# Kernel tuning notes

Hardware: AMD Instinct MI355X
Metric: run time of the kernel (lower is better)

The kernel has to match this reference:

```python
import jax, jax.numpy as jnp
import numpy as np

B, NUM_CLASSES, G = 8, 80, 100
IMG = 1280
STRIDES = (8, 16, 32)
EPS = 1e-7            # mmyolo EPS in -log(iou + EPS)
IOU_EPS = 1e-6        # BboxOverlaps2D union eps
INF = 1e8
SOFT_CENTER_RADIUS = 3.0
TOPK = 13
IOU_WEIGHT = 3.0


def _make_priors():
    ps = []
    for s in STRIDES:
        n = IMG // s
        c = (jnp.arange(n, dtype=jnp.float32) + 0.5) * s
        yy, xx = jnp.meshgrid(c, c, indexing='ij')
        st = jnp.full((n * n,), float(s), jnp.float32)
        ps.append(jnp.stack([xx.ravel(), yy.ravel(), st, st], axis=-1))
    return jnp.concatenate(ps, axis=0)  # [N, 4] = (cx, cy, stride_x, stride_y)


def setup_inputs() -> dict:
    key = jax.random.key(0)
    k = jax.random.split(key, 8)
    priors = _make_priors()
    N = priors.shape[0]  # 33600
    # predicted boxes jittered around anchor points, xyxy
    cxcy = priors[None, :, :2] + jax.random.normal(k[0], (B, N, 2)) * priors[None, :, 2:3] * 2.0
    wh = priors[None, :, 2:3] * (1.0 + 4.0 * jax.random.uniform(k[1], (B, N, 2)))
    pred_bboxes = jnp.concatenate([cxcy - wh / 2, cxcy + wh / 2], axis=-1)
    pred_scores = jax.random.normal(k[2], (B, N, NUM_CLASSES)) * 2.0 - 2.0  # logits
    # gt boxes inside the image, xyxy
    x1y1 = jax.random.uniform(k[3], (B, G, 2)) * (IMG - 200)
    gwh = 20.0 + jax.random.uniform(k[4], (B, G, 2)) * 180.0
    gt_bboxes = jnp.concatenate([x1y1, x1y1 + gwh], axis=-1)
    gt_labels = jax.random.randint(k[5], (B, G, 1), 0, NUM_CLASSES)
    counts = jax.random.randint(k[6], (B,), 10, G + 1)
    pad_bbox_flag = (jnp.arange(G)[None, :] < counts[:, None]).astype(jnp.float32)[..., None]
    return {"pred_bboxes": pred_bboxes, "pred_scores": pred_scores, "priors": priors,
            "gt_labels": gt_labels, "gt_bboxes": gt_bboxes, "pad_bbox_flag": pad_bbox_flag}


def _pairwise_iou(b1, b2):
    # b1 [B,N,4], b2 [B,G,4] in xyxy -> [B,N,G]
    a1 = (b1[..., 2] - b1[..., 0]) * (b1[..., 3] - b1[..., 1])
    a2 = (b2[..., 2] - b2[..., 0]) * (b2[..., 3] - b2[..., 1])
    lt = jnp.maximum(b1[:, :, None, :2], b2[:, None, :, :2])
    rb = jnp.minimum(b1[:, :, None, 2:], b2[:, None, :, 2:])
    wh = jnp.clip(rb - lt, 0.0)
    overlap = wh[..., 0] * wh[..., 1]
    union = a1[:, :, None] + a2[:, None, :] - overlap
    return overlap / jnp.maximum(union, IOU_EPS)


def reference(pred_bboxes, pred_scores, priors, gt_labels, gt_bboxes, pad_bbox_flag):
    Bb, N, _ = pred_bboxes.shape
    Gg = gt_bboxes.shape[1]
    centers = priors[:, :2]
    valid_gt = pad_bbox_flag[..., 0] > 0  # [B,G]

    # point-in-box test (strict >0, as in find_inside_points)
    lt = centers[None, :, None, :] - gt_bboxes[:, None, :, :2]   # [B,N,G,2]
    rb = gt_bboxes[:, None, :, 2:] - centers[None, :, None, :]
    is_in = (jnp.minimum(jnp.min(lt, -1), jnp.min(rb, -1)) > 0) & valid_gt[:, None, :]
    valid_mask = jnp.any(is_in, -1)  # [B,N]

    # soft center prior
    gt_center = (gt_bboxes[..., :2] + gt_bboxes[..., 2:]) / 2.0
    strides = priors[:, 2]
    dist = jnp.sqrt(jnp.sum((centers[None, :, None, :] - gt_center[:, None, :, :]) ** 2, -1))
    dist = dist / strides[None, :, None] * valid_mask[..., None].astype(dist.dtype)
    soft_center_prior = jnp.power(10.0, dist - SOFT_CENTER_RADIUS)

    # IoU cost
    ious = _pairwise_iou(pred_bboxes, gt_bboxes)  # [B,N,G]
    iou_cost = -jnp.log(ious + EPS) * IOU_WEIGHT

    # classification cost: gather pred score of each gt's class
    lbl = jnp.broadcast_to(gt_labels[:, None, :, 0], (Bb, N, Gg))
    x = jnp.take_along_axis(pred_scores, lbl, axis=2)  # logits [B,N,G]
    scale = ious - jax.nn.sigmoid(x)
    bce = jax.nn.softplus(x) - x * ious  # BCE-with-logits, target=ious
    cls_cost = bce * (scale * scale)

    cost = cls_cost + iou_cost + soft_center_prior
    cost = jnp.where(valid_mask[..., None], cost, INF)

    # dynamic k per gt = clamp(int(sum of top-13 ious), min 1)
    k = min(TOPK, N)
    topk_ious = jax.lax.top_k(jnp.swapaxes(ious, 1, 2), k)[0]  # [B,G,k]
    dyn_k = jnp.maximum(jnp.sum(topk_ious, -1).astype(jnp.int32), 1)  # [B,G]

    # rank of each prior's cost within its gt column (ascending)
    ranks = jnp.argsort(jnp.argsort(cost, axis=1), axis=1)
    matching = (ranks < dyn_k[:, None, :]) & valid_gt[:, None, :]  # [B,N,G]

    # resolve priors matched to multiple gts: keep min-cost gt
    multi = jnp.sum(matching, -1) > 1  # [B,N]
    argmin_g = jnp.argmin(cost, axis=-1)
    onehot = argmin_g[..., None] == jnp.arange(Gg)[None, None, :]
    matching = jnp.where(multi[..., None], onehot, matching)

    fg = jnp.any(matching, -1)                       # [B,N]
    matched_gt = jnp.argmax(matching, -1)            # [B,N]
    matched_ious = jnp.sum(jnp.where(matching, ious, 0.0), -1)

    lbls = jnp.take_along_axis(gt_labels[..., 0], matched_gt, axis=1)
    assigned_labels = jnp.where(fg, lbls, NUM_CLASSES)
    assigned_labels_weights = jnp.ones((Bb, N), pred_scores.dtype)
    boxes = jnp.take_along_axis(gt_bboxes, matched_gt[..., None], axis=1)
    assigned_bboxes = jnp.where(fg[..., None], boxes, 0.0)
    assign_metrics = jnp.where(fg, matched_ious, 0.0)
    return assigned_labels, assigned_labels_weights, assigned_bboxes, assign_metrics
```

## Files before the change

kernel.cpp:

```cpp
#include <hip/hip_runtime.h>
#include <stdint.h>

#define BDIM 256
#define TDIM 512
#define B_   8
#define NCLS 80
#define G_   100
#define N_   33600
#define TOPK_ 13
#define TILES 525
#define NW   8
#define CAPC 160
#define CAPI 160
#define INFC 1e8f


__device__ __forceinline__ unsigned int fkey(float f){
  unsigned int u = __float_as_uint(f);
  return (u & 0x80000000u) ? ~u : (u | 0x80000000u);
}
__device__ __forceinline__ float unfkey(unsigned int k){
  unsigned int u = (k & 0x80000000u) ? (k & 0x7fffffffu) : ~k;
  return __uint_as_float(u);
}

__device__ __forceinline__ float cost_eval(float iou, float x, float dist, bool valid){
  #pragma clang fp contract(off)
  float prior = exp2f((dist - 3.0f) * 3.321928094887362f);
  float iouc  = -logf(iou + 1e-7f) * 3.0f;
  float sig   = 1.0f / (1.0f + expf(-x));
  float sc    = iou - sig;
  float bce   = fmaxf(x, 0.0f) + log1pf(expf(-fabsf(x))) - x * iou;
  float c     = bce * (sc * sc) + iouc + prior;
  return valid ? c : INFC;
}

__device__ __forceinline__ unsigned long long wave_min_u64(unsigned long long v){
  #pragma unroll
  for (int m = 1; m < 64; m <<= 1){
    unsigned int lo = (unsigned int)__shfl_xor((int)(unsigned int)v, m, 64);
    unsigned int hi = (unsigned int)__shfl_xor((int)(unsigned int)(v >> 32), m, 64);
    unsigned long long o = ((unsigned long long)hi << 32) | lo;
    v = o < v ? o : v;
  }
  return v;
}

__device__ __forceinline__ void tile_params(int t, int& W, int& base, int& trow, int& tcol,
                                            float& s, float& invs){
  if (t < 400){            W = 160; base = 0;     s = 8.0f;  invs = 0.125f;
    trow = (t/20)*8;  tcol = (t - (t/20)*20)*8; }
  else if (t < 500){ int u = t - 400; W = 80; base = 25600; s = 16.0f; invs = 0.0625f;
    trow = (u/10)*8; tcol = (u - (u/10)*10)*8; }
  else {             int u = t - 500; W = 40; base = 32000; s = 32.0f; invs = 0.03125f;
    trow = (u/5)*8;  tcol = (u - (u/5)*5)*8; }
}

__device__ unsigned long long compact_cost(unsigned long long* buf, int cnt){
  const int lane = threadIdx.x & 63;
  unsigned long long a0 = (lane       < cnt) ? buf[lane]       : ~0ull;
  unsigned long long a1 = (lane + 64  < cnt) ? buf[lane + 64]  : ~0ull;
  unsigned long long a2 = (lane + 128 < cnt) ? buf[lane + 128] : ~0ull;
  unsigned long long mykeep = ~0ull, t13 = ~0ull;
  #pragma unroll
  for (int r = 0; r < TOPK_; ++r){
    unsigned long long v = a0 < a1 ? a0 : a1; v = v < a2 ? v : a2;
    unsigned long long mn = wave_min_u64(v);
    if      (a0 == mn) a0 = ~0ull;
    else if (a1 == mn) a1 = ~0ull;
    else if (a2 == mn) a2 = ~0ull;
    if (lane == r) mykeep = mn;
    t13 = mn;
  }
  if (lane < TOPK_) buf[lane] = mykeep;
  return t13;
}

__device__ float compact_iou(float* buf, int cnt){
  const int lane = threadIdx.x & 63;
  float a0 = (lane       < cnt) ? buf[lane]       : -1.0f;
  float a1 = (lane + 64  < cnt) ? buf[lane + 64]  : -1.0f;
  float a2 = (lane + 128 < cnt) ? buf[lane + 128] : -1.0f;
  float mykeep = -1.0f, t13 = -1.0f;
  #pragma unroll
  for (int r = 0; r < TOPK_; ++r){
    float mx = fmaxf(fmaxf(a0, a1), a2);
    #pragma unroll
    for (int m = 1; m < 64; m <<= 1) mx = fmaxf(mx, __shfl_xor(mx, m, 64));
    bool h0 = (a0 == mx), h1 = (a1 == mx), h2 = (a2 == mx);
    unsigned long long ball = __ballot(h0 | h1 | h2);
    int src = (int)(__ffsll(ball) - 1);
    if (lane == src){
      if (h0) a0 = -1.0f; else if (h1) a1 = -1.0f; else a2 = -1.0f;
    }
    if (lane == r) mykeep = mx;
    t13 = mx;
  }
  if (lane < TOPK_) buf[lane] = mykeep;
  return t13;
}


__global__ void __launch_bounds__(64) k_prep(
    const float* __restrict__ pred_bboxes,
    const float* __restrict__ gt_bboxes,
    const float* __restrict__ pad_flag,
    unsigned char* __restrict__ valid_mask,
    uint32_t* __restrict__ match_mask,
    float4* __restrict__ tile_agg,
    uint32_t* __restrict__ tile_flag)
{
  const int t = blockIdx.x, b = blockIdx.y, l = threadIdx.x;
  __shared__ float4 sbox[G_];
  __shared__ float  sflag[G_];
  for (int g = l; g < G_; g += 64){
    sbox[g]  = ((const float4*)gt_bboxes)[b*G_ + g];
    sflag[g] = pad_flag[b*G_ + g];
  }
  __syncthreads();

  int W, base, trow, tcol; float s, invs;
  tile_params(t, W, base, trow, tcol, s, invs);
  int row = trow + (l >> 3), col = tcol + (l & 7);
  int n = base + row*W + col;
  float cx = ((float)col + 0.5f)*s, cy = ((float)row + 0.5f)*s;

  bool v = false;
  for (int g = 0; g < G_; ++g){
    float4 gb = sbox[g];
    bool in = (cx - gb.x > 0.0f) & (cy - gb.y > 0.0f) &
              (gb.z - cx > 0.0f) & (gb.w - cy > 0.0f) & (sflag[g] > 0.0f);
    v |= in;
  }
  size_t idx = (size_t)b*N_ + n;
  valid_mask[idx] = v ? 1 : 0;
  ((uint4*)match_mask)[idx] = make_uint4(0u,0u,0u,0u);

  float4 pb = ((const float4*)pred_bboxes)[idx];
  float x1 = pb.x, y1 = pb.y, x2 = pb.z, y2 = pb.w;
  #pragma unroll
  for (int m = 1; m < 64; m <<= 1){
    x1 = fminf(x1, __shfl_xor(x1, m, 64));
    y1 = fminf(y1, __shfl_xor(y1, m, 64));
    x2 = fmaxf(x2, __shfl_xor(x2, m, 64));
    y2 = fmaxf(y2, __shfl_xor(y2, m, 64));
  }
  unsigned long long anyb = __ballot(v);
  if (l == 0){
    tile_agg [(size_t)b*TILES + t] = make_float4(x1, y1, x2, y2);
    tile_flag[(size_t)b*TILES + t] = (anyb != 0ull) ? 1u : 0u;
  }
}


__global__ void __launch_bounds__(TDIM) k_topk(
    const float* __restrict__ pred_bboxes,
    const float* __restrict__ pred_scores,
    const int*   __restrict__ gt_labels,
    const float* __restrict__ gt_bboxes,
    const float* __restrict__ pad_flag,
    const unsigned char* __restrict__ valid_mask,
    const float4* __restrict__ tile_agg,
    const uint32_t* __restrict__ tile_flag,
    uint32_t* __restrict__ match_mask)
{
  #pragma clang fp contract(off)
  const int g = blockIdx.x, b = blockIdx.y;
  if (pad_flag[b*G_ + g] <= 0.0f) return;

  __shared__ unsigned long long s_cbuf[NW][CAPC];
  __shared__ float s_ibuf[NW][CAPI];
  __shared__ unsigned long long s_fk[NW*TOPK_];
  __shared__ float s_fi[NW*TOPK_];
  __shared__ float s_thr[2];

  const int tid = threadIdx.x, lane = tid & 63, wid = tid >> 6;
  unsigned long long* cbuf = s_cbuf[wid];
  float* ibuf = s_ibuf[wid];

  const float4 gb = ((const float4*)gt_bboxes)[b*G_ + g];
  const float ga  = (gb.z - gb.x) * (gb.w - gb.y);
  const float gcx = (gb.x + gb.z) * 0.5f, gcy = (gb.y + gb.w) * 0.5f;
  const int lbl = gt_labels[b*G_ + g];
  const unsigned int KEYINF = fkey(INFC);

  const float4* pb4 = (const float4*)pred_bboxes + (size_t)b*N_;
  const unsigned char* vm = valid_mask + (size_t)b*N_;
  const float* sc_b = pred_scores + (size_t)b*N_*NCLS;
  const float4* tag = tile_agg + (size_t)b*TILES;
  const uint32_t* tfl = tile_flag + (size_t)b*TILES;

  if (wid == 0){
    auto seed_eval = [&](int t, float& cst, float& iouv){
      #pragma clang fp contract(off)
      int nk, bs; float s, invs;
      if      (t < 25){ nk = 160; bs = 0;     s = 8.0f;  invs = 0.125f;   }
      else if (t < 50){ nk = 80;  bs = 25600; s = 16.0f; invs = 0.0625f;  }
      else            { nk = 40;  bs = 32000; s = 32.0f; invs = 0.03125f; }
      int rem = (t < 25) ? t : ((t < 50) ? t - 25 : t - 50);
      int r = rem / 5, c = rem - 5*r;
      int ix = (int)(gcx / s) - 2, iy = (int)(gcy / s) - 2;
      ix = ix < 0 ? 0 : (ix > nk-5 ? nk-5 : ix);
      iy = iy < 0 ? 0 : (iy > nk-5 ? nk-5 : iy);
      int col = ix + c, row = iy + r;
      int n = bs + row*nk + col;
      float4 pb = pb4[n];
      float pa = (pb.z - pb.x) * (pb.w - pb.y);
      float lx = fmaxf(pb.x, gb.x), ly = fmaxf(pb.y, gb.y);
      float rx = fminf(pb.z, gb.z), ry = fminf(pb.w, gb.w);
      float ov = fmaxf(rx - lx, 0.0f) * fmaxf(ry - ly, 0.0f);
      float un = pa + ga - ov;
      float iou = ov / fmaxf(un, 1e-6f);
      iouv = iou;
      bool valid = vm[n] != 0;
      float px = ((float)col + 0.5f)*s, py = ((float)row + 0.5f)*s;
      float dx = px - gcx, dy = py - gcy;
      float dist = sqrtf(dx*dx + dy*dy) * invs;
      float x = valid ? sc_b[(size_t)n*NCLS + lbl] : 0.0f;
      cst = cost_eval(iou, x, dist, valid);
    };
    float c0 = 3e38f, c1 = 3e38f, i0 = -1.0f, i1 = -1.0f;
    seed_eval(lane, c0, i0);
    if (lane < 11) seed_eval(lane + 64, c1, i1);
    float T = INFC;
    {
      const float lvs[7] = {47.0f, 24.0f, 12.0f, 6.0f, 3.0f, 1.5f, 0.75f};
      #pragma unroll
      for (int i = 0; i < 7; ++i){
        int cnt = __popcll(__ballot(c0 <= lvs[i])) + __popcll(__ballot(c1 <= lvs[i]));
        if (cnt >= TOPK_) T = lvs[i];
      }
    }
    float Ti = 0.0f;
    {
      const float ivs[8] = {0.02f, 0.05f, 0.1f, 0.15f, 0.22f, 0.3f, 0.4f, 0.5f};
      #pragma unroll
      for (int i = 0; i < 8; ++i){
        int cnt = __popcll(__ballot(i0 >= ivs[i])) + __popcll(__ballot(i1 >= ivs[i]));
        if (cnt >= TOPK_) Ti = ivs[i] * 0.999f;
      }
    }
    if (lane == 0){ s_thr[0] = T; s_thr[1] = Ti; }
  }
  __syncthreads();

  const float T0 = s_thr[0];
  float Tiou_m = s_thr[1];
  unsigned long long Tkey = ((unsigned long long)fkey(T0) << 32) | 0xFFFFFFFFull;
  bool  tc48  = T0 < 48.0f;
  float gt_   = 3.02f + log10f(T0);
  float gthr2 = gt_ * gt_;

  int ccnt = 0, icnt = 0;

  int sweep_nend = 0;
  if (T0 == INFC){
    int found = 0, base = 0;
    while (found < TOPK_ && base < N_){
      int n = base + lane;
      bool inv = (vm[n] == 0);
      unsigned long long m = __ballot(inv);
      int pc = __popcll(m);
      if (wid == 0){
        int pos = ccnt + (int)__popcll(m & ((1ull << lane) - 1ull));
        if (inv) cbuf[pos] = ((unsigned long long)KEYINF << 32) | (unsigned)n;
        ccnt += pc;
      }
      found += pc;
      base += 64;
    }
    sweep_nend = base;
  }

  const int per  = (TILES + NW - 1) / NW;
  const int lo_w = wid*per;
  const int hi_w = min(TILES, lo_w + per);

  for (int tb = lo_w; tb < hi_w; tb += 64){
    int tt2 = tb + lane;
    bool pass = false;
    if (tt2 < hi_w){
      float4 ag = tag[tt2];
      uint32_t fl2 = tfl[tt2];
      int W, bse, trow, tcol; float s, invs;
      tile_params(tt2, W, bse, trow, tcol, s, invs);
      bool inter = (fminf(ag.z, gb.z) > fmaxf(ag.x, gb.x)) &&
                   (fminf(ag.w, gb.w) > fmaxf(ag.y, gb.y));
      float rx0 = ((float)tcol + 0.5f)*s, rx1 = ((float)tcol + 7.5f)*s;
      float ry0 = ((float)trow + 0.5f)*s, ry1 = ((float)trow + 7.5f)*s;
      float ddx = fmaxf(0.0f, fmaxf(rx0 - gcx, gcx - rx1));
      float ddy = fmaxf(0.0f, fmaxf(ry0 - gcy, gcy - ry1));
      float md2s = (ddx*ddx + ddy*ddy) * (invs*invs);
      bool costok = (fl2 != 0) && (md2s <= gthr2) && (inter || !tc48);
      pass = inter || costok;
    }
    unsigned long long pm = __ballot(pass);
    while (pm){
      int bit = (int)(__ffsll(pm) - 1);
      pm &= pm - 1ull;
      const int tt = tb + bit;

      int W, bse, trow, tcol; float s, invs;
      tile_params(tt, W, bse, trow, tcol, s, invs);
      int row = trow + (lane >> 3), col = tcol + (lane & 7);
      int n = bse + row*W + col;
      float px = ((float)col + 0.5f)*s, py = ((float)row + 0.5f)*s;
      float4 pb = pb4[n];
      float pa = (pb.z - pb.x) * (pb.w - pb.y);
      float lx = fmaxf(pb.x, gb.x), ly = fmaxf(pb.y, gb.y);
      float rx = fminf(pb.z, gb.z), ry = fminf(pb.w, gb.w);
      float ov = fmaxf(rx - lx, 0.0f) * fmaxf(ry - ly, 0.0f);
      float un = pa + ga - ov;
      bool ipass = ov > Tiou_m * un;

      float dx = px - gcx, dy = py - gcy;
      float dist2 = dx*dx + dy*dy;
      float d2s = dist2 * (invs * invs);
      bool valid = vm[n] != 0;
      bool needcost = valid && (d2s <= gthr2) && !((ov <= 0.0f) && tc48);

      float iou = 0.0f;
      if (__any(ipass || needcost)){
        if (ipass || needcost) iou = ov / fmaxf(un, 1e-6f);
      }

      {
        unsigned long long m = __ballot(ipass);
        if (m){
          int pc = __popcll(m);
          if (icnt + pc > CAPI){
            float t = compact_iou(ibuf, icnt); icnt = TOPK_;
            Tiou_m = t * 0.999f;
          }
          int pos = icnt + (int)__popcll(m & ((1ull << lane) - 1ull));
          if (ipass) ibuf[pos] = iou;
          icnt += pc;
        }
      }

      unsigned long long key = ((unsigned long long)KEYINF << 32) | (unsigned)n;
      bool cpass = (!valid) && (key < Tkey) && (n >= sweep_nend);
      if (__any(needcost)){
        if (needcost){
          float x = sc_b[(size_t)n*NCLS + lbl];
          float dist = sqrtf(dist2) * invs;
          float c = cost_eval(iou, x, dist, true);
          key = ((unsigned long long)fkey(c) << 32) | (unsigned)n;
          cpass = key < Tkey;
        }
      }
      {
        unsigned long long m = __ballot(cpass);
        if (m){
          int pc = __popcll(m);
          if (ccnt + pc > CAPC){
            Tkey = compact_cost(cbuf, ccnt); ccnt = TOPK_;
            float Tc = unfkey((unsigned int)(Tkey >> 32));
            tc48 = Tc < 48.0f;
            float gq = 3.02f + log10f(Tc);
            gthr2 = (gq > 0.0f) ? gq*gq : 1e30f;
          }
          int pos = ccnt + (int)__popcll(m & ((1ull << lane) - 1ull));
          if (cpass) cbuf[pos] = key;
          ccnt += pc;
        }
      }
    }
  }

  compact_cost(cbuf, ccnt);
  compact_iou(ibuf, icnt);
  if (lane < TOPK_){ s_fk[wid*TOPK_ + lane] = cbuf[lane]; s_fi[wid*TOPK_ + lane] = ibuf[lane]; }
  __syncthreads();

  if (wid == 0){
    compact_cost(s_fk, NW*TOPK_);
    compact_iou(s_fi, NW*TOPK_);
  }
  __syncthreads();

  if (tid == 0){
    float ssum = 0.0f;
    for (int r = 0; r < TOPK_; ++r) ssum += fmaxf(s_fi[r], 0.0f);
    int dynk = (int)ssum;
    if (dynk < 1) dynk = 1;
    if (dynk > TOPK_) dynk = TOPK_;
    for (int r = 0; r < dynk; ++r){
      int n = (int)(s_fk[r] & 0xffffffffu);
      if (n < N_)
        atomicOr(&match_mask[((size_t)b*N_ + n)*4 + (g >> 5)], 1u << (g & 31));
    }
  }
}


__global__ void __launch_bounds__(BDIM) k_assign(
    const float* __restrict__ pred_bboxes,
    const float* __restrict__ pred_scores,
    const float* __restrict__ priors,
    const int*   __restrict__ gt_labels,
    const float* __restrict__ gt_bboxes,
    const unsigned char* __restrict__ valid_mask,
    const uint32_t* __restrict__ match_mask,
    float* __restrict__ out)
{
  #pragma clang fp contract(off)
  const int b = blockIdx.y;
  __shared__ float4 sbox[G_];
  __shared__ int    slbl[G_];
  __shared__ float  sga[G_], sgcx[G_], sgcy[G_];
  for (int g = threadIdx.x; g < G_; g += BDIM){
    float4 q = ((const float4*)gt_bboxes)[b*G_ + g];
    sbox[g] = q; slbl[g] = gt_labels[b*G_ + g];
    sga[g]  = (q.z - q.x) * (q.w - q.y);
    sgcx[g] = (q.x + q.z) * 0.5f;
    sgcy[g] = (q.y + q.w) * 0.5f;
  }
  __syncthreads();
  int n = blockIdx.x*BDIM + threadIdx.x;
  if (n >= N_) return;
  const int lane = threadIdx.x & 63;
  size_t idx = (size_t)b*N_ + n;
  uint4 mm = ((const uint4*)match_mask)[idx];
  int count = __popc(mm.x) + __popc(mm.y) + __popc(mm.z) + __popc(mm.w);

  float lblv = (float)NCLS;
  float4 ob = make_float4(0.f, 0.f, 0.f, 0.f);
  float met = 0.0f;

  if (__any(count > 0)){
    float4 pb = make_float4(0.f,0.f,0.f,0.f); float pa = 0.0f;
    if (count > 0){
      pb = ((const float4*)pred_bboxes)[idx];
      pa = (pb.z - pb.x) * (pb.w - pb.y);
    }
    if (count == 1){
      int mg = mm.x ? (__ffs(mm.x) - 1) :
               mm.y ? (31 + __ffs(mm.y)) :
               mm.z ? (63 + __ffs(mm.z)) : (95 + __ffs(mm.w));
      float4 q = sbox[mg];
      float lx = fmaxf(pb.x, q.x), ly = fmaxf(pb.y, q.y);
      float rx = fminf(pb.z, q.z), ry = fminf(pb.w, q.w);
      float ov = fmaxf(rx - lx, 0.0f) * fmaxf(ry - ly, 0.0f);
      float iou = ov / fmaxf(pa + sga[mg] - ov, 1e-6f);
      lblv = (float)slbl[mg]; ob = q; met = iou;
    }
    unsigned long long heavy = __ballot(count > 1);
    if (heavy){
      float4 pr = make_float4(0.f,0.f,0.f,0.f); int hv0 = 0;
      if (count > 1){
        pr = ((const float4*)priors)[n];
        hv0 = valid_mask[idx];
      }
      while (heavy){
        int src = (int)(__ffsll(heavy) - 1);
        heavy &= heavy - 1ull;
        float hx1 = __shfl(pb.x, src, 64), hy1 = __shfl(pb.y, src, 64);
        float hx2 = __shfl(pb.z, src, 64), hy2 = __shfl(pb.w, src, 64);
        float hpa = __shfl(pa,   src, 64);
        float hcx = __shfl(pr.x, src, 64), hcy = __shfl(pr.y, src, 64);
        float hst = __shfl(pr.z, src, 64);
        int   hv  = __shfl(hv0,  src, 64);
        int   hn  = __shfl(n,    src, 64);
        float hinvs = __uint_as_float(0x7F000000u - __float_as_uint(hst));
        const float* hrow = pred_scores + ((size_t)b*N_ + hn)*(size_t)NCLS;

        unsigned long long bk = ~0ull;
        #pragma unroll
        for (int h = 0; h < 2; ++h){
          int g = lane + h*64;
          if (g < G_){
            float4 q = sbox[g];
            float lx = fmaxf(hx1, q.x), ly = fmaxf(hy1, q.y);
            float rx = fminf(hx2, q.z), ry = fminf(hy2, q.w);
            float ov = fmaxf(rx - lx, 0.0f) * fmaxf(ry - ly, 0.0f);
            float un = hpa + sga[g] - ov;
            float iou = ov / fmaxf(un, 1e-6f);
            float dx = hcx - sgcx[g], dy = hcy - sgcy[g];
            float dist = sqrtf(dx*dx + dy*dy) * hinvs;
            float x = hrow[slbl[g]];
            float c = cost_eval(iou, x, dist, hv != 0);
            unsigned long long key = ((unsigned long long)fkey(c) << 32) | (unsigned)g;
            bk = key < bk ? key : bk;
          }
        }
        bk = wave_min_u64(bk);
        if (lane == src){
          int gw = (int)(bk & 0xffffffffu);
          float4 q = sbox[gw];
          float lx = fmaxf(pb.x, q.x), ly = fmaxf(pb.y, q.y);
          float rx = fminf(pb.z, q.z), ry = fminf(pb.w, q.w);
          float ov = fmaxf(rx - lx, 0.0f) * fmaxf(ry - ly, 0.0f);
          met  = ov / fmaxf(pa + sga[gw] - ov, 1e-6f);
          lblv = (float)slbl[gw];
          ob = q;
        }
      }
    }
  }

  out[idx] = lblv;
  out[(size_t)B_*N_ + idx] = 1.0f;
  ((float4*)(out + (size_t)2*B_*N_))[idx] = ob;
  out[(size_t)6*B_*N_ + idx] = met;
}


extern "C" void kernel_launch(void* const* d_in, const int* in_sizes, int n_in,
                              void* d_out, int out_size, void* d_ws, size_t ws_size,
                              hipStream_t stream) {
  const float* pred_bboxes = (const float*)d_in[0];
  const float* pred_scores = (const float*)d_in[1];
  const float* priors      = (const float*)d_in[2];
  const int*   gt_labels   = (const int*)  d_in[3];
  const float* gt_bboxes   = (const float*)d_in[4];
  const float* pad_flag    = (const float*)d_in[5];
  float* out = (float*)d_out;

  const size_t MASK_B  = (size_t)B_*N_*4*sizeof(uint32_t);
  const size_t VALID_B = ((size_t)B_*N_ + 255) & ~(size_t)255;
  const size_t AGG_B   = (size_t)B_*TILES*sizeof(float4);
  uint32_t* match_mask = (uint32_t*)d_ws;
  unsigned char* valid_mask = (unsigned char*)d_ws + MASK_B;
  float4* tile_agg = (float4*)((char*)d_ws + MASK_B + VALID_B);
  uint32_t* tile_flag = (uint32_t*)((char*)d_ws + MASK_B + VALID_B + AGG_B);

  dim3 gridT(TILES, B_);
  dim3 gridG(G_, B_);
  dim3 gridN((N_ + BDIM - 1)/BDIM, B_);

  k_prep<<<gridT, 64, 0, stream>>>(pred_bboxes, gt_bboxes, pad_flag,
                                   valid_mask, match_mask, tile_agg, tile_flag);
  k_topk<<<gridG, TDIM, 0, stream>>>(pred_bboxes, pred_scores, gt_labels,
                                     gt_bboxes, pad_flag, valid_mask,
                                     tile_agg, tile_flag, match_mask);
  k_assign<<<gridN, BDIM, 0, stream>>>(pred_bboxes, pred_scores, priors, gt_labels,
                                       gt_bboxes, valid_mask, match_mask, out);
}
```

Baseline: 72.86 us.

## Balance tile work across waves with shared work queue and parallel seeding

In k_topk, tile filtering is now done by all threads into a shared list of passing tiles. Waves pull tiles dynamically through an atomic counter instead of each wave owning a static contiguous range, which evens out load when passing tiles cluster near the gt box. Seed threshold evaluation is spread across all eight waves using shared atomic histograms rather than run on wave 0 alone. k_prep packs four tiles per 256-thread block to cut the number of tiny blocks. The cost is extra shared-memory atomics and barriers.

```diff
diff --git a/kernel.cpp b/kernel.cpp
--- a/kernel.cpp
+++ b/kernel.cpp
@@ -101,7 +101,7 @@
 }
 
 
-__global__ void __launch_bounds__(64) k_prep(
+__global__ void __launch_bounds__(BDIM) k_prep(
     const float* __restrict__ pred_bboxes,
     const float* __restrict__ gt_bboxes,
     const float* __restrict__ pad_flag,
@@ -110,18 +110,20 @@
     float4* __restrict__ tile_agg,
     uint32_t* __restrict__ tile_flag)
 {
-  const int t = blockIdx.x, b = blockIdx.y, l = threadIdx.x;
+  const int b = blockIdx.y, tid = threadIdx.x, lane = tid & 63, wid = tid >> 6;
+  const int t = blockIdx.x*4 + wid;
   __shared__ float4 sbox[G_];
   __shared__ float  sflag[G_];
-  for (int g = l; g < G_; g += 64){
+  for (int g = tid; g < G_; g += BDIM){
     sbox[g]  = ((const float4*)gt_bboxes)[b*G_ + g];
     sflag[g] = pad_flag[b*G_ + g];
   }
   __syncthreads();
+  if (t >= TILES) return;
 
   int W, base, trow, tcol; float s, invs;
   tile_params(t, W, base, trow, tcol, s, invs);
-  int row = trow + (l >> 3), col = tcol + (l & 7);
+  int row = trow + (lane >> 3), col = tcol + (lane & 7);
   int n = base + row*W + col;
   float cx = ((float)col + 0.5f)*s, cy = ((float)row + 0.5f)*s;
 
@@ -146,7 +148,7 @@
     y2 = fmaxf(y2, __shfl_xor(y2, m, 64));
   }
   unsigned long long anyb = __ballot(v);
-  if (l == 0){
+  if (lane == 0){
     tile_agg [(size_t)b*TILES + t] = make_float4(x1, y1, x2, y2);
     tile_flag[(size_t)b*TILES + t] = (anyb != 0ull) ? 1u : 0u;
   }
@@ -172,6 +174,9 @@
   __shared__ float s_ibuf[NW][CAPI];
   __shared__ unsigned long long s_fk[NW*TOPK_];
   __shared__ float s_fi[NW*TOPK_];
+  __shared__ unsigned short s_list[TILES];
+  __shared__ int s_np, s_pop;
+  __shared__ int s_ccnt[7], s_icnt[8];
   __shared__ float s_thr[2];
 
   const int tid = threadIdx.x, lane = tid & 63, wid = tid >> 6;
@@ -190,7 +195,12 @@
   const float4* tag = tile_agg + (size_t)b*TILES;
   const uint32_t* tfl = tile_flag + (size_t)b*TILES;
 
-  if (wid == 0){
+  if (tid < 7) s_ccnt[tid] = 0;
+  if (tid < 8) s_icnt[tid] = 0;
+  if (tid == 0){ s_np = 0; s_pop = 0; }
+  __syncthreads();
+
+  {
     auto seed_eval = [&](int t, float& cst, float& iouv){
       #pragma clang fp contract(off)
       int nk, bs; float s, invs;
@@ -219,28 +229,33 @@
       float x = valid ? sc_b[(size_t)n*NCLS + lbl] : 0.0f;
       cst = cost_eval(iou, x, dist, valid);
     };
-    float c0 = 3e38f, c1 = 3e38f, i0 = -1.0f, i1 = -1.0f;
-    seed_eval(lane, c0, i0);
-    if (lane < 11) seed_eval(lane + 64, c1, i1);
-    float T = INFC;
-    {
-      const float lvs[7] = {47.0f, 24.0f, 12.0f, 6.0f, 3.0f, 1.5f, 0.75f};
-      #pragma unroll
-      for (int i = 0; i < 7; ++i){
-        int cnt = __popcll(__ballot(c0 <= lvs[i])) + __popcll(__ballot(c1 <= lvs[i]));
-        if (cnt >= TOPK_) T = lvs[i];
-      }
-    }
-    float Ti = 0.0f;
-    {
-      const float ivs[8] = {0.02f, 0.05f, 0.1f, 0.15f, 0.22f, 0.3f, 0.4f, 0.5f};
-      #pragma unroll
-      for (int i = 0; i < 8; ++i){
-        int cnt = __popcll(__ballot(i0 >= ivs[i])) + __popcll(__ballot(i1 >= ivs[i]));
-        if (cnt >= TOPK_) Ti = ivs[i] * 0.999f;
-      }
-    }
-    if (lane == 0){ s_thr[0] = T; s_thr[1] = Ti; }
+    float cv = 3e38f, iv = -1.0f;
+    int e = wid*10 + lane;
+    bool act = (lane < 10) && (e < 75);
+    if (act) seed_eval(e, cv, iv);
+    const float lvs[7] = {47.0f, 24.0f, 12.0f, 6.0f, 3.0f, 1.5f, 0.75f};
+    #pragma unroll
+    for (int i = 0; i < 7; ++i){
+      int cnt = __popcll(__ballot(act && (cv <= lvs[i])));
+      if (lane == 0 && cnt) atomicAdd(&s_ccnt[i], cnt);
+    }
+    const float ivs[8] = {0.02f, 0.05f, 0.1f, 0.15f, 0.22f, 0.3f, 0.4f, 0.5f};
+    #pragma unroll
+    for (int i = 0; i < 8; ++i){
+      int cnt = __popcll(__ballot(act && (iv >= ivs[i])));
+      if (lane == 0 && cnt) atomicAdd(&s_icnt[i], cnt);
+    }
+  }
+  __syncthreads();
+  if (tid == 0){
+    const float lvs[7] = {47.0f, 24.0f, 12.0f, 6.0f, 3.0f, 1.5f, 0.75f};
+    const float ivs[8] = {0.02f, 0.05f, 0.1f, 0.15f, 0.22f, 0.3f, 0.4f, 0.5f};
+    float T = INFC, Ti = 0.0f;
+    #pragma unroll
+    for (int i = 0; i < 7; ++i) if (s_ccnt[i] >= TOPK_) T = lvs[i];
+    #pragma unroll
+    for (int i = 0; i < 8; ++i) if (s_icnt[i] >= TOPK_) Ti = ivs[i] * 0.999f;
+    s_thr[0] = T; s_thr[1] = Ti;
   }
   __syncthreads();
 
@@ -272,98 +287,97 @@
     sweep_nend = base;
   }
 
-  const int per  = (TILES + NW - 1) / NW;
-  const int lo_w = wid*per;
-  const int hi_w = min(TILES, lo_w + per);
-
-  for (int tb = lo_w; tb < hi_w; tb += 64){
-    int tt2 = tb + lane;
-    bool pass = false;
-    if (tt2 < hi_w){
-      float4 ag = tag[tt2];
-      uint32_t fl2 = tfl[tt2];
-      int W, bse, trow, tcol; float s, invs;
-      tile_params(tt2, W, bse, trow, tcol, s, invs);
-      bool inter = (fminf(ag.z, gb.z) > fmaxf(ag.x, gb.x)) &&
-                   (fminf(ag.w, gb.w) > fmaxf(ag.y, gb.y));
-      float rx0 = ((float)tcol + 0.5f)*s, rx1 = ((float)tcol + 7.5f)*s;
-      float ry0 = ((float)trow + 0.5f)*s, ry1 = ((float)trow + 7.5f)*s;
-      float ddx = fmaxf(0.0f, fmaxf(rx0 - gcx, gcx - rx1));
-      float ddy = fmaxf(0.0f, fmaxf(ry0 - gcy, gcy - ry1));
-      float md2s = (ddx*ddx + ddy*ddy) * (invs*invs);
-      bool costok = (fl2 != 0) && (md2s <= gthr2) && (inter || !tc48);
-      pass = inter || costok;
-    }
-    unsigned long long pm = __ballot(pass);
-    while (pm){
-      int bit = (int)(__ffsll(pm) - 1);
-      pm &= pm - 1ull;
-      const int tt = tb + bit;
-
-      int W, bse, trow, tcol; float s, invs;
-      tile_params(tt, W, bse, trow, tcol, s, invs);
-      int row = trow + (lane >> 3), col = tcol + (lane & 7);
-      int n = bse + row*W + col;
-      float px = ((float)col + 0.5f)*s, py = ((float)row + 0.5f)*s;
-      float4 pb = pb4[n];
-      float pa = (pb.z - pb.x) * (pb.w - pb.y);
-      float lx = fmaxf(pb.x, gb.x), ly = fmaxf(pb.y, gb.y);
-      float rx = fminf(pb.z, gb.z), ry = fminf(pb.w, gb.w);
-      float ov = fmaxf(rx - lx, 0.0f) * fmaxf(ry - ly, 0.0f);
-      float un = pa + ga - ov;
-      bool ipass = ov > Tiou_m * un;
-
-      float dx = px - gcx, dy = py - gcy;
-      float dist2 = dx*dx + dy*dy;
-      float d2s = dist2 * (invs * invs);
-      bool valid = vm[n] != 0;
-      bool needcost = valid && (d2s <= gthr2) && !((ov <= 0.0f) && tc48);
-
-      float iou = 0.0f;
-      if (__any(ipass || needcost)){
-        if (ipass || needcost) iou = ov / fmaxf(un, 1e-6f);
+  for (int t = tid; t < TILES; t += TDIM){
+    float4 ag = tag[t];
+    uint32_t fl2 = tfl[t];
+    int W, bse, trow, tcol; float s, invs;
+    tile_params(t, W, bse, trow, tcol, s, invs);
+    bool inter = (fminf(ag.z, gb.z) > fmaxf(ag.x, gb.x)) &&
+                 (fminf(ag.w, gb.w) > fmaxf(ag.y, gb.y));
+    float rx0 = ((float)tcol + 0.5f)*s, rx1 = ((float)tcol + 7.5f)*s;
+    float ry0 = ((float)trow + 0.5f)*s, ry1 = ((float)trow + 7.5f)*s;
+    float ddx = fmaxf(0.0f, fmaxf(rx0 - gcx, gcx - rx1));
+    float ddy = fmaxf(0.0f, fmaxf(ry0 - gcy, gcy - ry1));
+    float md2s = (ddx*ddx + ddy*ddy) * (invs*invs);
+    bool costok = (fl2 != 0) && (md2s <= gthr2) && (inter || !tc48);
+    if (inter || costok){
+      int p = atomicAdd(&s_np, 1);
+      s_list[p] = (unsigned short)t;
+    }
+  }
+  __syncthreads();
+  const int npass = s_np;
+
+  for (;;){
+    int widx = 0;
+    if (lane == 0) widx = atomicAdd(&s_pop, 1);
+    widx = __shfl(widx, 0, 64);
+    if (widx >= npass) break;
+    const int tt = s_list[widx];
+
+    int W, bse, trow, tcol; float s, invs;
+    tile_params(tt, W, bse, trow, tcol, s, invs);
+    int row = trow + (lane >> 3), col = tcol + (lane & 7);
+    int n = bse + row*W + col;
+    float px = ((float)col + 0.5f)*s, py = ((float)row + 0.5f)*s;
+    float4 pb = pb4[n];
+    float pa = (pb.z - pb.x) * (pb.w - pb.y);
+    float lx = fmaxf(pb.x, gb.x), ly = fmaxf(pb.y, gb.y);
+    float rx = fminf(pb.z, gb.z), ry = fminf(pb.w, gb.w);
+    float ov = fmaxf(rx - lx, 0.0f) * fmaxf(ry - ly, 0.0f);
+    float un = pa + ga - ov;
+    bool ipass = ov > Tiou_m * un;
+
+    float dx = px - gcx, dy = py - gcy;
+    float dist2 = dx*dx + dy*dy;
+    float d2s = dist2 * (invs * invs);
+    bool valid = vm[n] != 0;
+    bool needcost = valid && (d2s <= gthr2) && !((ov <= 0.0f) && tc48);
+
+    float iou = 0.0f;
+    if (__any(ipass || needcost)){
+      if (ipass || needcost) iou = ov / fmaxf(un, 1e-6f);
+    }
+
+    {
+      unsigned long long m = __ballot(ipass);
+      if (m){
+        int pc = __popcll(m);
+        if (icnt + pc > CAPI){
+          float t = compact_iou(ibuf, icnt); icnt = TOPK_;
+          Tiou_m = t * 0.999f;
+        }
+        int pos = icnt + (int)__popcll(m & ((1ull << lane) - 1ull));
+        if (ipass) ibuf[pos] = iou;
+        icnt += pc;
       }
-
-      {
-        unsigned long long m = __ballot(ipass);
-        if (m){
-          int pc = __popcll(m);
-          if (icnt + pc > CAPI){
-            float t = compact_iou(ibuf, icnt); icnt = TOPK_;
-            Tiou_m = t * 0.999f;
-          }
-          int pos = icnt + (int)__popcll(m & ((1ull << lane) - 1ull));
-          if (ipass) ibuf[pos] = iou;
-          icnt += pc;
+    }
+
+    unsigned long long key = ((unsigned long long)KEYINF << 32) | (unsigned)n;
+    bool cpass = (!valid) && (key < Tkey) && (n >= sweep_nend);
+    if (__any(needcost)){
+      if (needcost){
+        float x = sc_b[(size_t)n*NCLS + lbl];
+        float dist = sqrtf(dist2) * invs;
+        float c = cost_eval(iou, x, dist, true);
+        key = ((unsigned long long)fkey(c) << 32) | (unsigned)n;
+        cpass = key < Tkey;
+      }
+    }
+    {
+      unsigned long long m = __ballot(cpass);
+      if (m){
+        int pc = __popcll(m);
+        if (ccnt + pc > CAPC){
+          Tkey = compact_cost(cbuf, ccnt); ccnt = TOPK_;
+          float Tc = unfkey((unsigned int)(Tkey >> 32));
+          tc48 = Tc < 48.0f;
+          float gq = 3.02f + log10f(Tc);
+          gthr2 = (gq > 0.0f) ? gq*gq : 1e30f;
         }
-      }
-
-      unsigned long long key = ((unsigned long long)KEYINF << 32) | (unsigned)n;
-      bool cpass = (!valid) && (key < Tkey) && (n >= sweep_nend);
-      if (__any(needcost)){
-        if (needcost){
-          float x = sc_b[(size_t)n*NCLS + lbl];
-          float dist = sqrtf(dist2) * invs;
-          float c = cost_eval(iou, x, dist, true);
-          key = ((unsigned long long)fkey(c) << 32) | (unsigned)n;
-          cpass = key < Tkey;
-        }
-      }
-      {
-        unsigned long long m = __ballot(cpass);
-        if (m){
-          int pc = __popcll(m);
-          if (ccnt + pc > CAPC){
-            Tkey = compact_cost(cbuf, ccnt); ccnt = TOPK_;
-            float Tc = unfkey((unsigned int)(Tkey >> 32));
-            tc48 = Tc < 48.0f;
-            float gq = 3.02f + log10f(Tc);
-            gthr2 = (gq > 0.0f) ? gq*gq : 1e30f;
-          }
-          int pos = ccnt + (int)__popcll(m & ((1ull << lane) - 1ull));
-          if (cpass) cbuf[pos] = key;
-          ccnt += pc;
-        }
+        int pos = ccnt + (int)__popcll(m & ((1ull << lane) - 1ull));
+        if (cpass) cbuf[pos] = key;
+        ccnt += pc;
       }
     }
   }
@@ -525,12 +539,12 @@
   float4* tile_agg = (float4*)((char*)d_ws + MASK_B + VALID_B);
   uint32_t* tile_flag = (uint32_t*)((char*)d_ws + MASK_B + VALID_B + AGG_B);
 
-  dim3 gridT(TILES, B_);
+  dim3 gridT((TILES + 3)/4, B_);
   dim3 gridG(G_, B_);
   dim3 gridN((N_ + BDIM - 1)/BDIM, B_);
 
-  k_prep<<<gridT, 64, 0, stream>>>(pred_bboxes, gt_bboxes, pad_flag,
-                                   valid_mask, match_mask, tile_agg, tile_flag);
+  k_prep<<<gridT, BDIM, 0, stream>>>(pred_bboxes, gt_bboxes, pad_flag,
+                                     valid_mask, match_mask, tile_agg, tile_flag);
   k_topk<<<gridG, TDIM, 0, stream>>>(pred_bboxes, pred_scores, gt_labels,
                                      gt_bboxes, pad_flag, valid_mask,
                                      tile_agg, tile_flag, match_mask);
```

Result: slower. 87.68 us (+20.3%).

## Split per-gt top-k search across two chunks and merge in a separate kernel

Applied to the files above, without the earlier changes.

The top-k kernel grid gains a chunk dimension, so each gt's tile range is split in half across two blocks that each write their partial top-13 cost keys and IoUs to workspace. A new merge kernel combines the two sorted partial lists, computes dynamic k, and sets the match mask bits. The prep kernel also packs four tiles per 256-thread block instead of one tile per 64-thread block. This doubles block-level parallelism for the top-k stage at the cost of an extra launch, extra workspace traffic, and a single-threaded serial merge.

```diff
diff --git a/kernel.cpp b/kernel.cpp
--- a/kernel.cpp
+++ b/kernel.cpp
@@ -10,6 +10,7 @@
 #define TOPK_ 13
 #define TILES 525
 #define NW   8
+#define NCHUNK 2
 #define CAPC 160
 #define CAPI 160
 #define INFC 1e8f
@@ -101,7 +102,7 @@
 }
 
 
-__global__ void __launch_bounds__(64) k_prep(
+__global__ void __launch_bounds__(BDIM) k_prep(
     const float* __restrict__ pred_bboxes,
     const float* __restrict__ gt_bboxes,
     const float* __restrict__ pad_flag,
@@ -110,18 +111,20 @@
     float4* __restrict__ tile_agg,
     uint32_t* __restrict__ tile_flag)
 {
-  const int t = blockIdx.x, b = blockIdx.y, l = threadIdx.x;
+  const int b = blockIdx.y, tid = threadIdx.x, lane = tid & 63, wid = tid >> 6;
+  const int t = blockIdx.x*4 + wid;
   __shared__ float4 sbox[G_];
   __shared__ float  sflag[G_];
-  for (int g = l; g < G_; g += 64){
+  for (int g = tid; g < G_; g += BDIM){
     sbox[g]  = ((const float4*)gt_bboxes)[b*G_ + g];
     sflag[g] = pad_flag[b*G_ + g];
   }
   __syncthreads();
+  if (t >= TILES) return;
 
   int W, base, trow, tcol; float s, invs;
   tile_params(t, W, base, trow, tcol, s, invs);
-  int row = trow + (l >> 3), col = tcol + (l & 7);
+  int row = trow + (lane >> 3), col = tcol + (lane & 7);
   int n = base + row*W + col;
   float cx = ((float)col + 0.5f)*s, cy = ((float)row + 0.5f)*s;
 
@@ -146,7 +149,7 @@
     y2 = fmaxf(y2, __shfl_xor(y2, m, 64));
   }
   unsigned long long anyb = __ballot(v);
-  if (l == 0){
+  if (lane == 0){
     tile_agg [(size_t)b*TILES + t] = make_float4(x1, y1, x2, y2);
     tile_flag[(size_t)b*TILES + t] = (anyb != 0ull) ? 1u : 0u;
   }
@@ -162,10 +165,11 @@
     const unsigned char* __restrict__ valid_mask,
     const float4* __restrict__ tile_agg,
     const uint32_t* __restrict__ tile_flag,
-    uint32_t* __restrict__ match_mask)
+    unsigned long long* __restrict__ ck_out,
+    float* __restrict__ ci_out)
 {
   #pragma clang fp contract(off)
-  const int g = blockIdx.x, b = blockIdx.y;
+  const int g = blockIdx.x, b = blockIdx.y, chunk = blockIdx.z;
   if (pad_flag[b*G_ + g] <= 0.0f) return;
 
   __shared__ unsigned long long s_cbuf[NW][CAPC];
@@ -261,7 +265,7 @@
       bool inv = (vm[n] == 0);
       unsigned long long m = __ballot(inv);
       int pc = __popcll(m);
-      if (wid == 0){
+      if (chunk == 0 && wid == 0){
         int pos = ccnt + (int)__popcll(m & ((1ull << lane) - 1ull));
         if (inv) cbuf[pos] = ((unsigned long long)KEYINF << 32) | (unsigned)n;
         ccnt += pc;
@@ -272,9 +276,12 @@
     sweep_nend = base;
   }
 
-  const int per  = (TILES + NW - 1) / NW;
-  const int lo_w = wid*per;
-  const int hi_w = min(TILES, lo_w + per);
+  const int per = (TILES + NW - 1) / NW;
+  const int lo_full = wid*per;
+  const int hi_full = min(TILES, lo_full + per);
+  const int half = (hi_full - lo_full + 1) >> 1;
+  const int lo_w = lo_full + (chunk ? half : 0);
+  const int hi_w = chunk ? hi_full : (lo_full + half);
 
   for (int tb = lo_w; tb < hi_w; tb += 64){
     int tt2 = tb + lane;
@@ -379,17 +386,49 @@
   }
   __syncthreads();
 
-  if (tid == 0){
-    float ssum = 0.0f;
-    for (int r = 0; r < TOPK_; ++r) ssum += fmaxf(s_fi[r], 0.0f);
-    int dynk = (int)ssum;
-    if (dynk < 1) dynk = 1;
-    if (dynk > TOPK_) dynk = TOPK_;
-    for (int r = 0; r < dynk; ++r){
-      int n = (int)(s_fk[r] & 0xffffffffu);
-      if (n < N_)
-        atomicOr(&match_mask[((size_t)b*N_ + n)*4 + (g >> 5)], 1u << (g & 31));
-    }
+  if (tid < TOPK_){
+    size_t base = (((size_t)b*G_ + g)*NCHUNK + chunk)*TOPK_;
+    ck_out[base + tid] = s_fk[tid];
+    ci_out[base + tid] = s_fi[tid];
+  }
+}
+
+
+__global__ void __launch_bounds__(64) k_merge(
+    const float* __restrict__ pad_flag,
+    const unsigned long long* __restrict__ ck,
+    const float* __restrict__ ci,
+    uint32_t* __restrict__ match_mask)
+{
+  const int g = blockIdx.x, b = blockIdx.y;
+  if (threadIdx.x != 0) return;
+  if (pad_flag[b*G_ + g] <= 0.0f) return;
+
+  const size_t base = ((size_t)b*G_ + g)*NCHUNK*TOPK_;
+  const unsigned long long* K = ck + base;
+  const float* I = ci + base;
+
+  int p0 = 0, p1 = 0; float s = 0.0f;
+  for (int r = 0; r < TOPK_; ++r){
+    float v0 = (p0 < TOPK_) ? I[p0]         : -1e30f;
+    float v1 = (p1 < TOPK_) ? I[TOPK_ + p1] : -1e30f;
+    float mx = fmaxf(v0, v1);
+    if (v0 == mx) p0++; else p1++;
+    s += fmaxf(mx, 0.0f);
+  }
+  int dynk = (int)s;
+  if (dynk < 1) dynk = 1;
+  if (dynk > TOPK_) dynk = TOPK_;
+
+  int q0 = 0, q1 = 0;
+  for (int r = 0; r < dynk; ++r){
+    unsigned long long k0 = (q0 < TOPK_) ? K[q0]         : ~0ull;
+    unsigned long long k1 = (q1 < TOPK_) ? K[TOPK_ + q1] : ~0ull;
+    unsigned long long mn = k0 < k1 ? k0 : k1;
+    if (k0 == mn) q0++; else q1++;
+    int n = (int)(mn & 0xffffffffu);
+    if (n < N_)
+      atomicOr(&match_mask[((size_t)b*N_ + n)*4 + (g >> 5)], 1u << (g & 31));
   }
 }
 
@@ -519,21 +558,27 @@
 
   const size_t MASK_B  = (size_t)B_*N_*4*sizeof(uint32_t);
   const size_t VALID_B = ((size_t)B_*N_ + 255) & ~(size_t)255;
+  const size_t CK_B    = (size_t)B_*G_*NCHUNK*TOPK_*sizeof(unsigned long long);
+  const size_t CI_B    = (size_t)B_*G_*NCHUNK*TOPK_*sizeof(float);
   const size_t AGG_B   = (size_t)B_*TILES*sizeof(float4);
   uint32_t* match_mask = (uint32_t*)d_ws;
   unsigned char* valid_mask = (unsigned char*)d_ws + MASK_B;
-  float4* tile_agg = (float4*)((char*)d_ws + MASK_B + VALID_B);
-  uint32_t* tile_flag = (uint32_t*)((char*)d_ws + MASK_B + VALID_B + AGG_B);
-
-  dim3 gridT(TILES, B_);
-  dim3 gridG(G_, B_);
+  unsigned long long* ck = (unsigned long long*)((char*)d_ws + MASK_B + VALID_B);
+  float* ci = (float*)((char*)d_ws + MASK_B + VALID_B + CK_B);
+  float4* tile_agg = (float4*)((char*)d_ws + MASK_B + VALID_B + CK_B + CI_B);
+  uint32_t* tile_flag = (uint32_t*)((char*)d_ws + MASK_B + VALID_B + CK_B + CI_B + AGG_B);
+
+  dim3 gridT((TILES + 3)/4, B_);
+  dim3 gridG(G_, B_, NCHUNK);
+  dim3 gridM(G_, B_);
   dim3 gridN((N_ + BDIM - 1)/BDIM, B_);
 
-  k_prep<<<gridT, 64, 0, stream>>>(pred_bboxes, gt_bboxes, pad_flag,
-                                   valid_mask, match_mask, tile_agg, tile_flag);
+  k_prep<<<gridT, BDIM, 0, stream>>>(pred_bboxes, gt_bboxes, pad_flag,
+                                     valid_mask, match_mask, tile_agg, tile_flag);
   k_topk<<<gridG, TDIM, 0, stream>>>(pred_bboxes, pred_scores, gt_labels,
                                      gt_bboxes, pad_flag, valid_mask,
-                                     tile_agg, tile_flag, match_mask);
+                                     tile_agg, tile_flag, ck, ci);
+  k_merge<<<gridM, 64, 0, stream>>>(pad_flag, ck, ci, match_mask);
   k_assign<<<gridN, BDIM, 0, stream>>>(pred_bboxes, pred_scores, priors, gt_labels,
                                        gt_bboxes, valid_mask, match_mask, out);
 }
```

After: 98.90 us. 1.36x slower.
